# Kernel optimization log

Measured on AMD Instinct MI355X. Metric: run time of the kernel, lower is better.

Reference implementation:

```python
import jax, jax.numpy as jnp
import numpy as np

B, S, HID = 2, 2048, 2048
H, K, D = 32, 8, 64          # query heads, kv heads, head_dim
G = H // K                   # GQA group size
ROPE_MSCALE = 1.2            # constant rope_mscale applied to q and k
SM_SCALE = 1.0 / (D ** 0.5)  # flash_attn default softmax scale


def rotate_half(x):
    h = x.shape[-1] // 2
    return jnp.concatenate([-x[..., h:], x[..., :h]], axis=-1)


def setup_inputs() -> dict:
    key = jax.random.key(0)
    k1, k2, k3, k4 = jax.random.split(key, 4)
    hidden_states = jax.random.normal(k1, (B, S, HID), dtype=jnp.float32)
    # standard rotary tables: cos/sin of shape [S, D]
    inv_freq = 1.0 / (10000.0 ** (jnp.arange(0, D, 2, dtype=jnp.float32) / D))
    freqs = jnp.outer(jnp.arange(S, dtype=jnp.float32), inv_freq)  # [S, D/2]
    emb = jnp.concatenate([freqs, freqs], axis=-1)                 # [S, D]
    cos, sin = jnp.cos(emb), jnp.sin(emb)
    per_head_scale = 1.0 + 0.1 * jax.random.normal(k2, (B, H), dtype=jnp.float32)
    Wqkv = jax.random.normal(k3, ((H + 2 * K) * D, HID), dtype=jnp.float32) * (HID ** -0.5)
    Wo = jax.random.normal(k4, (HID, H * D), dtype=jnp.float32) * ((H * D) ** -0.5)
    return {"cos": cos, "sin": sin, "hidden_states": hidden_states,
            "per_head_scale": per_head_scale, "Wqkv": Wqkv, "Wo": Wo}


def reference(cos, sin, hidden_states, per_head_scale, Wqkv, Wo):
    # fused QKV projection (CastedLinear, no bias)
    qkv = jnp.einsum('bsh,oh->bso', hidden_states, Wqkv)          # [B,S,(H+2K)*D]
    qkv = qkv.reshape(B, S, H + 2 * K, D)
    q = qkv[:, :, :H]                 # [B,S,H,D]
    k = qkv[:, :, H:H + K]            # [B,S,K,D]
    v = qkv[:, :, H + K:]             # [B,S,K,D]
    # rotary embedding: cos/sin [S,D] -> broadcast over heads via [S,1,D]
    c = cos[:, None, :]
    s_ = sin[:, None, :]
    q = q * c + rotate_half(q) * s_
    k = k * c + rotate_half(k) * s_
    # rope_mscale
    q = q * ROPE_MSCALE
    k = k * ROPE_MSCALE
    # per-head scale on queries: [B,H] -> [B,1,H,1]
    q = q * per_head_scale[:, None, :, None]
    # GQA attention without materializing repeated K/V: group query heads
    qg = q.reshape(B, S, K, G, D)
    scores = jnp.einsum('bqkgd,bskd->bkgqs', qg, k) * SM_SCALE    # [B,K,G,Sq,Sk]
    causal = jnp.arange(S)[:, None] >= jnp.arange(S)[None, :]     # [Sq,Sk]
    scores = jnp.where(causal, scores, jnp.finfo(scores.dtype).min)
    probs = jax.nn.softmax(scores, axis=-1)
    out = jnp.einsum('bkgqs,bskd->bqkgd', probs, v).reshape(B, S, H * D)
    return jnp.einsum('bso,ho->bsh', out, Wo)                     # o_proj
```

## Files before the change

kernel.cpp:

```cpp
#include <hip/hip_runtime.h>
#include <stdint.h>

typedef unsigned short u16;
typedef short short8 __attribute__((ext_vector_type(8)));
typedef float f32x4 __attribute__((ext_vector_type(4)));
typedef uint32_t u32x4 __attribute__((ext_vector_type(4)));

#define S_LEN 2048
#define NQH 32
#define NKH 8
#define DHD 64
#define MNEG -1.0e30f

__device__ __forceinline__ float b2f(u16 u){
  union { uint32_t i; float f; } c; c.i = ((uint32_t)u) << 16; return c.f;
}
__device__ __forceinline__ u16 f2b(float f){
  union { float f; uint32_t i; } c; c.f = f;
  uint32_t r = c.i + 0x7fffu + ((c.i >> 16) & 1u);
  return (u16)(r >> 16);
}
__device__ __forceinline__ uint32_t cvt_pk_bf16(float lo, float hi){
  uint32_t r;
  asm("v_cvt_pk_bf16_f32 %0, %1, %2" : "=v"(r) : "v"(lo), "v"(hi));
  return r;
}
__device__ __forceinline__ void gload_lds16(const void* g, void* l){
  __builtin_amdgcn_global_load_lds((const __attribute__((address_space(1))) uint32_t*)g,
                                   (__attribute__((address_space(3))) uint32_t*)l, 16, 0, 0);
}

__global__ __launch_bounds__(256) void cvt_all(const float* __restrict__ hs,
                                               const float* __restrict__ wq,
                                               const float* __restrict__ wo,
                                               u16* __restrict__ hsB,
                                               u16* __restrict__ wqB,
                                               u16* __restrict__ woB){
  int i = blockIdx.x * 256 + threadIdx.x;
  const float* src; u16* dst; int off;
  if (i < 2097152)      { src = hs; dst = hsB; off = i; }
  else if (i < 3670016) { src = wq; dst = wqB; off = i - 2097152; }
  else                  { src = wo; dst = woB; off = i - 3670016; }
  float4 v = ((const float4*)src)[off];
  uint2 o;
  o.x = (uint32_t)f2b(v.x) | ((uint32_t)f2b(v.y) << 16);
  o.y = (uint32_t)f2b(v.z) | ((uint32_t)f2b(v.w) << 16);
  ((uint2*)dst)[off] = o;
}

template<int OUT_F32>
__global__ __launch_bounds__(256)
void gemm_bt(const u16* __restrict__ A, const u16* __restrict__ Bm,
             void* __restrict__ Cp, int N, int K)
{
  __shared__ alignas(16) u16 lA[128 * 64];
  __shared__ alignas(16) u16 lB[128 * 64];
  const int tid = threadIdx.x;
  const int w = tid >> 6, l = tid & 63;
  const int lg = l >> 4, lc = l & 15;
  const int wm = w >> 1, wn = w & 1;
  const int m0 = blockIdx.y * 128, n0 = blockIdx.x * 128;
  const int srow = l >> 3, sc = l & 7;
  const size_t ldb = (size_t)K * 2;
  f32x4 acc[4][4] = {};
  const int kiters = K >> 6;
  for (int kt = 0; kt < kiters; ++kt){
    __syncthreads();
#pragma unroll
    for (int i = 0; i < 4; ++i){
      const int row = (i * 4 + w) * 8 + srow;
      const int gc = ((sc ^ (row & 7)) << 4);
      gload_lds16((const char*)A + (size_t)(m0 + row) * ldb + (size_t)kt * 128 + gc,
                  (char*)lA + row * 128 + sc * 16);
    }
#pragma unroll
    for (int i = 0; i < 4; ++i){
      const int row = (i * 4 + w) * 8 + srow;
      const int gc = ((sc ^ (row & 7)) << 4);
      gload_lds16((const char*)Bm + (size_t)(n0 + row) * ldb + (size_t)kt * 128 + gc,
                  (char*)lB + row * 128 + sc * 16);
    }
    __syncthreads();
#pragma unroll
    for (int kk = 0; kk < 2; ++kk){
      short8 af[4], bfr[4];
#pragma unroll
      for (int mi = 0; mi < 4; ++mi){
        const int row = wm * 64 + mi * 16 + lc;
        const int cc = (kk * 4 + lg) ^ (row & 7);
        af[mi] = *(const short8*)((const char*)lA + row * 128 + cc * 16);
      }
#pragma unroll
      for (int ni = 0; ni < 4; ++ni){
        const int row = wn * 64 + ni * 16 + lc;
        const int cc = (kk * 4 + lg) ^ (row & 7);
        bfr[ni] = *(const short8*)((const char*)lB + row * 128 + cc * 16);
      }
#pragma unroll
      for (int mi = 0; mi < 4; ++mi)
#pragma unroll
        for (int ni = 0; ni < 4; ++ni)
          acc[mi][ni] = __builtin_amdgcn_mfma_f32_16x16x32_bf16(af[mi], bfr[ni], acc[mi][ni], 0, 0, 0);
    }
  }
  const int r0 = m0 + wm * 64 + lg * 4;
  const int c0 = n0 + wn * 64 + lc;
#pragma unroll
  for (int mi = 0; mi < 4; ++mi)
#pragma unroll
    for (int ni = 0; ni < 4; ++ni)
#pragma unroll
      for (int j = 0; j < 4; ++j){
        const size_t idx = (size_t)(r0 + mi * 16 + j) * (size_t)N + (size_t)(c0 + ni * 16);
        if (OUT_F32) ((float*)Cp)[idx] = acc[mi][ni][j];
        else         ((u16*)Cp)[idx]  = f2b(acc[mi][ni][j]);
      }
}

__global__ __launch_bounds__(256)
void rope_kernel(const u16* __restrict__ qkv, const float* __restrict__ cosT,
                 const float* __restrict__ sinT, const float* __restrict__ phs,
                 u16* __restrict__ Qo, u16* __restrict__ Ko)
{
  int id = blockIdx.x * 256 + threadIdx.x;
  int b = (id >= 327680) ? 1 : 0;
  int rem = id - b * 327680;
  int head = rem >> 13;
  int s = (rem >> 2) & 2047;
  int d0 = (rem & 3) << 4;
  const u16* src = qkv + (((size_t)(b * S_LEN + s) * 48 + head) << 6);
  uint4 xa = *(const uint4*)(src + d0);
  uint4 xb = *(const uint4*)(src + d0 + 8);
  int d0p = (d0 + 32) & 63;
  uint4 pa = *(const uint4*)(src + d0p);
  uint4 pb = *(const uint4*)(src + d0p + 8);
  const float* cp = cosT + s * 64 + d0;
  const float* sp = sinT + s * 64 + d0;
  const float sgn = (d0 < 32) ? -1.f : 1.f;
  const float kscale = 0.18033688011112042f;
  const float scale = (head < NQH) ? 1.2f * kscale * phs[b * NQH + head] : 1.2f;
  uint32_t xs[4] = {xa.x, xa.y, xa.z, xa.w};
  uint32_t xs2[4] = {xb.x, xb.y, xb.z, xb.w};
  uint32_t ps[4] = {pa.x, pa.y, pa.z, pa.w};
  uint32_t ps2[4] = {pb.x, pb.y, pb.z, pb.w};
  uint32_t ow[8];
#pragma unroll
  for (int k = 0; k < 4; ++k){
    float v0 = b2f((u16)(xs[k] & 0xffff)) * cp[2*k]   + sgn * b2f((u16)(ps[k] & 0xffff)) * sp[2*k];
    float v1 = b2f((u16)(xs[k] >> 16))    * cp[2*k+1] + sgn * b2f((u16)(ps[k] >> 16))    * sp[2*k+1];
    ow[k] = (uint32_t)f2b(v0 * scale) | ((uint32_t)f2b(v1 * scale) << 16);
  }
#pragma unroll
  for (int k = 0; k < 4; ++k){
    float v0 = b2f((u16)(xs2[k] & 0xffff)) * cp[8+2*k]   + sgn * b2f((u16)(ps2[k] & 0xffff)) * sp[8+2*k];
    float v1 = b2f((u16)(xs2[k] >> 16))    * cp[8+2*k+1] + sgn * b2f((u16)(ps2[k] >> 16))    * sp[8+2*k+1];
    ow[4+k] = (uint32_t)f2b(v0 * scale) | ((uint32_t)f2b(v1 * scale) << 16);
  }
  u16* dst;
  if (head < NQH) dst = Qo + (((size_t)(b * NQH + head) * S_LEN + s) << 6) + d0;
  else            dst = Ko + (((size_t)(b * NKH + head - NQH) * S_LEN + s) << 6) + d0;
  uint4 o0 = {ow[0], ow[1], ow[2], ow[3]};
  uint4 o1 = {ow[4], ow[5], ow[6], ow[7]};
  *(uint4*)dst = o0;
  *(uint4*)(dst + 8) = o1;
}

__global__ __launch_bounds__(256)
void vtrans(const u16* __restrict__ qkv, u16* __restrict__ VT)
{
  int bid = blockIdx.x;
  int st = bid & 31, kh = (bid >> 5) & 7, b = bid >> 8;
  __shared__ alignas(16) u16 t[64][72];
  int tid = threadIdx.x;
  int r = tid >> 2, c4 = tid & 3;
  const u16* src = qkv + (((size_t)(b * S_LEN + st * 64 + r) * 48 + 40 + kh) << 6) + c4 * 16;
  *(uint4*)&t[r][c4 * 16]     = *(const uint4*)src;
  *(uint4*)&t[r][c4 * 16 + 8] = *(const uint4*)(src + 8);
  __syncthreads();
  u16 o[16];
#pragma unroll
  for (int i = 0; i < 16; ++i) o[i] = t[c4 * 16 + i][r];
  u16* dst = VT + ((size_t)(b * NKH + kh) * 64 + r) * S_LEN + st * 64 + c4 * 16;
  uint4 o0 = { (uint32_t)o[0] | ((uint32_t)o[1] << 16),  (uint32_t)o[2] | ((uint32_t)o[3] << 16),
               (uint32_t)o[4] | ((uint32_t)o[5] << 16),  (uint32_t)o[6] | ((uint32_t)o[7] << 16) };
  uint4 o1 = { (uint32_t)o[8] | ((uint32_t)o[9] << 16),  (uint32_t)o[10] | ((uint32_t)o[11] << 16),
               (uint32_t)o[12] | ((uint32_t)o[13] << 16),(uint32_t)o[14] | ((uint32_t)o[15] << 16) };
  *(uint4*)dst = o0;
  *(uint4*)(dst + 8) = o1;
}

__device__ __forceinline__ void proc_chunk(f32x4 (&sv)[8], float& mrow, float& lsum,
                                           f32x4 (&o)[4], uint32_t (&pw)[4][4],
                                           const int lg, const int lc,
                                           const bool diag, const int qloc)
{
  if (diag){
#pragma unroll
    for (int nj = 0; nj < 8; ++nj)
#pragma unroll
      for (int jj = 0; jj < 4; ++jj){
        const int kloc = nj * 16 + lg * 4 + jj;
        if (kloc > qloc) sv[nj][jj] = MNEG;
      }
  }
  float mu = sv[0][0];
#pragma unroll
  for (int nj = 0; nj < 8; ++nj)
#pragma unroll
    for (int jj = 0; jj < 4; ++jj) mu = fmaxf(mu, sv[nj][jj]);
  mu = fmaxf(mu, __shfl_xor(mu, 16));
  mu = fmaxf(mu, __shfl_xor(mu, 32));
  if (!__all(mu <= mrow + 11.54f)){
    const float mnew = fmaxf(mrow, mu);
    const float sf = __builtin_amdgcn_exp2f(mrow - mnew);
    mrow = mnew;
    lsum *= sf;
#pragma unroll
    for (int dn = 0; dn < 4; ++dn)
#pragma unroll
      for (int jj = 0; jj < 4; ++jj) o[dn][jj] *= sf;
  }
  const float mcur = mrow;
  float ps = 0.f;
#pragma unroll
  for (int nj = 0; nj < 8; ++nj)
#pragma unroll
    for (int jj = 0; jj < 4; ++jj){
      const float pv = __builtin_amdgcn_exp2f(sv[nj][jj] - mcur);
      sv[nj][jj] = pv;
      ps += pv;
    }
  lsum += ps;
  uint32_t rx[8], ry[8];
#pragma unroll
  for (int nj = 0; nj < 8; ++nj){
    rx[nj] = cvt_pk_bf16(sv[nj][0], sv[nj][1]);
    ry[nj] = cvt_pk_bf16(sv[nj][2], sv[nj][3]);
  }
  const int srcA = (lg & 1) * 32 + lc;
  const bool hi = (lg & 2) != 0;
#pragma unroll
  for (int kk2 = 0; kk2 < 4; ++kk2){
    uint32_t x0 = (uint32_t)__shfl((int)rx[kk2 * 2],     srcA);
    uint32_t x1 = (uint32_t)__shfl((int)rx[kk2 * 2 + 1], srcA);
    uint32_t y0 = (uint32_t)__shfl((int)ry[kk2 * 2],     srcA);
    uint32_t y1 = (uint32_t)__shfl((int)ry[kk2 * 2 + 1], srcA);
    pw[kk2][0] = hi ? x1 : x0;
    pw[kk2][1] = hi ? y1 : y0;
    x0 = (uint32_t)__shfl((int)rx[kk2 * 2],     srcA + 16);
    x1 = (uint32_t)__shfl((int)rx[kk2 * 2 + 1], srcA + 16);
    y0 = (uint32_t)__shfl((int)ry[kk2 * 2],     srcA + 16);
    y1 = (uint32_t)__shfl((int)ry[kk2 * 2 + 1], srcA + 16);
    pw[kk2][2] = hi ? x1 : x0;
    pw[kk2][3] = hi ? y1 : y0;
  }
}

__device__ __forceinline__ short8 pw_frag(const uint32_t* pw){
  u32x4 v = { pw[0], pw[1], pw[2], pw[3] };
  return __builtin_bit_cast(short8, v);
}

__global__ __launch_bounds__(512, 2)
void attn_kernel(const u16* __restrict__ Q, const u16* __restrict__ Kr,
                 const u16* __restrict__ VT, u16* __restrict__ Ao)
{
  int bid = blockIdx.x;
  int p  = bid & 15;
  int gp = (bid >> 4) & 1;
  int kh = (bid >> 5) & 7;
  int b  = bid >> 8;
  const int qt0 = p, qt1 = 31 - p;

  __shared__ alignas(16) u16 lK[2][128 * 64];
  __shared__ alignas(16) u16 lV[2][64 * 128];

  const int tid = threadIdx.x;
  const int hh = tid >> 8;
  const int h  = kh * 4 + gp * 2 + hh;
  const int w  = (tid >> 6) & 3;
  const int l  = tid & 63;
  const int lg = l >> 4, lc = l & 15;

  short8 qf[2][2];
  {
    const u16* qbase = Q + ((size_t)(b * NQH + h) * S_LEN) * 64;
#pragma unroll
    for (int kk = 0; kk < 2; ++kk){
      qf[0][kk] = *(const short8*)(qbase + (size_t)(qt0 * 64 + w * 16 + lc) * 64 + kk * 32 + lg * 8);
      qf[1][kk] = *(const short8*)(qbase + (size_t)(qt1 * 64 + w * 16 + lc) * 64 + kk * 32 + lg * 8);
    }
  }

  const u16* Kb = Kr + (size_t)(b * NKH + kh) * S_LEN * 64;
  const u16* Vb = VT + (size_t)(b * NKH + kh) * 64 * S_LEN;

  f32x4 o[2][4] = {};
  float mrow[2] = {MNEG, MNEG};
  float lsum[2] = {0.f, 0.f};

  const int nt = (qt1 >> 1) + 1;
  const int nt0 = qt0 >> 1;

#define STAGE(T, BSEL) do { \
    _Pragma("unroll") \
    for (int i_ = 0; i_ < 2; ++i_){ \
      const int row_ = i_ * 64 + (tid >> 3); \
      const int ch_  = tid & 7; \
      const int gc_  = ((ch_ ^ (row_ & 7)) << 4); \
      gload_lds16((const char*)(Kb + (size_t)((T) * 128 + row_) * 64) + gc_, \
                  (char*)lK[BSEL] + row_ * 128 + ch_ * 16); \
    } \
    _Pragma("unroll") \
    for (int i_ = 0; i_ < 2; ++i_){ \
      const int row_ = i_ * 32 + (tid >> 4); \
      const int ch_  = tid & 15; \
      const int gc_  = ((ch_ ^ (row_ & 15)) << 4); \
      gload_lds16((const char*)(Vb + (size_t)row_ * S_LEN + (T) * 128) + gc_, \
                  (char*)lV[BSEL] + row_ * 256 + ch_ * 16); \
    } \
  } while (0)

  STAGE(0, 0);

  for (int t = 0; t < nt; ++t){
    const int cur = t & 1;
    const bool act0 = (t <= nt0);
    if (t + 1 < nt){
      STAGE(t + 1, cur ^ 1);
      asm volatile("s_waitcnt vmcnt(4)" ::: "memory");
    } else {
      asm volatile("s_waitcnt vmcnt(0)" ::: "memory");
    }
    __builtin_amdgcn_s_barrier();

    f32x4 sv[2][8] = {};
    __builtin_amdgcn_s_setprio(1);
#pragma unroll
    for (int kk = 0; kk < 2; ++kk){
      short8 kf[8];
#pragma unroll
      for (int nj = 0; nj < 8; ++nj){
        const int row = nj * 16 + lc;
        const int cc = (kk * 4 + lg) ^ (row & 7);
        kf[nj] = *(const short8*)((const char*)lK[cur] + row * 128 + cc * 16);
      }
      if (act0)
#pragma unroll
        for (int nj = 0; nj < 8; ++nj)
          sv[0][nj] = __builtin_amdgcn_mfma_f32_16x16x32_bf16(kf[nj], qf[0][kk], sv[0][nj], 0, 0, 0);
#pragma unroll
      for (int nj = 0; nj < 8; ++nj)
        sv[1][nj] = __builtin_amdgcn_mfma_f32_16x16x32_bf16(kf[nj], qf[1][kk], sv[1][nj], 0, 0, 0);
    }
    __builtin_amdgcn_s_setprio(0);

    uint32_t pw[2][4][4];
    if (act0)
      proc_chunk(sv[0], mrow[0], lsum[0], o[0], pw[0], lg, lc,
                 t == (qt0 >> 1), (qt0 & 1) * 64 + w * 16 + lc);
    proc_chunk(sv[1], mrow[1], lsum[1], o[1], pw[1], lg, lc,
               t == (qt1 >> 1), (qt1 & 1) * 64 + w * 16 + lc);

    __builtin_amdgcn_s_setprio(1);
#pragma unroll
    for (int kk2 = 0; kk2 < 4; ++kk2){
      short8 vf[4];
#pragma unroll
      for (int dn = 0; dn < 4; ++dn){
        const int row = dn * 16 + lc;
        const int cc = (kk2 * 4 + lg) ^ (row & 15);
        vf[dn] = *(const short8*)((const char*)lV[cur] + row * 256 + cc * 16);
      }
      if (act0){
        const short8 pb0 = pw_frag(pw[0][kk2]);
#pragma unroll
        for (int dn = 0; dn < 4; ++dn)
          o[0][dn] = __builtin_amdgcn_mfma_f32_16x16x32_bf16(vf[dn], pb0, o[0][dn], 0, 0, 0);
      }
      const short8 pb1 = pw_frag(pw[1][kk2]);
#pragma unroll
      for (int dn = 0; dn < 4; ++dn)
        o[1][dn] = __builtin_amdgcn_mfma_f32_16x16x32_bf16(vf[dn], pb1, o[1][dn], 0, 0, 0);
    }
    __builtin_amdgcn_s_setprio(0);
    __builtin_amdgcn_s_barrier();
  }
#undef STAGE

#pragma unroll
  for (int c = 0; c < 2; ++c){
    const int qt = c ? qt1 : qt0;
    float ls = lsum[c];
    ls += __shfl_xor(ls, 16);
    ls += __shfl_xor(ls, 32);
    const float inv = 1.f / ls;
    const int sq = qt * 64 + w * 16 + lc;
#pragma unroll
    for (int dn = 0; dn < 4; ++dn){
      uint2 pk;
      pk.x = cvt_pk_bf16(o[c][dn][0] * inv, o[c][dn][1] * inv);
      pk.y = cvt_pk_bf16(o[c][dn][2] * inv, o[c][dn][3] * inv);
      const int col = h * 64 + dn * 16 + lg * 4;
      *(uint2*)&Ao[(size_t)(b * S_LEN + sq) * 2048 + col] = pk;
    }
  }
}

extern "C" void kernel_launch(void* const* d_in, const int* in_sizes, int n_in,
                              void* d_out, int out_size, void* d_ws, size_t ws_size,
                              hipStream_t stream)
{
  const float* cosT = (const float*)d_in[0];
  const float* sinT = (const float*)d_in[1];
  const float* hs   = (const float*)d_in[2];
  const float* phs  = (const float*)d_in[3];
  const float* Wqkv = (const float*)d_in[4];
  const float* Wo   = (const float*)d_in[5];
  float* out = (float*)d_out;
  char* ws = (char*)d_ws;

  u16* hsB   = (u16*)(ws);
  u16* WqkvB = (u16*)(ws + 16777216);
  u16* WoB   = (u16*)(ws + 29360128);
  u16* qkvB  = (u16*)(ws + 37748736);
  u16* Qb    = (u16*)(ws + 62914560);
  u16* Kb    = (u16*)(ws + 79691776);
  u16* VTb   = (u16*)(ws + 83886080);
  u16* Ao    = hsB;

  cvt_all<<<18432, 256, 0, stream>>>(hs, Wqkv, Wo, hsB, WqkvB, WoB);
  gemm_bt<0><<<dim3(24, 32), 256, 0, stream>>>(hsB, WqkvB, (void*)qkvB, 3072, 2048);
  rope_kernel<<<2560, 256, 0, stream>>>(qkvB, cosT, sinT, phs, Qb, Kb);
  vtrans<<<512, 256, 0, stream>>>(qkvB, VTb);
  attn_kernel<<<512, 512, 0, stream>>>(Qb, Kb, VTb, Ao);
  gemm_bt<1><<<dim3(16, 32), 256, 0, stream>>>(Ao, WoB, (void*)out, 2048, 2048);
}
```

Baseline: 237.6 us.

## Permute V^T key order to match P register layout, drop shuffles

The V transpose kernel now handles 128-key tiles and writes keys in a permuted order that matches the lane layout the softmax probabilities already have in registers. The attention inner loop then packs P to bf16 directly instead of doing 16 cross-lane shuffles per chunk. This removes shuffle and select work from the hot attention loop. The cost is a more complex, coordinated layout in the transpose kernel, and correctness depends on the permutation matching the MFMA fragment mapping exactly.

```diff
diff --git a/kernel.cpp b/kernel.cpp
--- a/kernel.cpp
+++ b/kernel.cpp
@@ -169,24 +169,36 @@
 void vtrans(const u16* __restrict__ qkv, u16* __restrict__ VT)
 {
   int bid = blockIdx.x;
-  int st = bid & 31, kh = (bid >> 5) & 7, b = bid >> 8;
-  __shared__ alignas(16) u16 t[64][72];
+  int t = bid & 15, kh = (bid >> 4) & 7, b = bid >> 7;
+  __shared__ u16 vlds[128][72];
   int tid = threadIdx.x;
-  int r = tid >> 2, c4 = tid & 3;
-  const u16* src = qkv + (((size_t)(b * S_LEN + st * 64 + r) * 48 + 40 + kh) << 6) + c4 * 16;
-  *(uint4*)&t[r][c4 * 16]     = *(const uint4*)src;
-  *(uint4*)&t[r][c4 * 16 + 8] = *(const uint4*)(src + 8);
+  {
+    int r = tid >> 1, half = tid & 1;
+    const u16* src = qkv + (((size_t)(b * S_LEN + t * 128 + r) * 48 + 40 + kh) << 6) + half * 32;
+    uint4 a0 = *(const uint4*)(src);
+    uint4 a1 = *(const uint4*)(src + 8);
+    uint4 a2 = *(const uint4*)(src + 16);
+    uint4 a3 = *(const uint4*)(src + 24);
+    *(uint4*)&vlds[r][half * 32]      = a0;
+    *(uint4*)&vlds[r][half * 32 + 8]  = a1;
+    *(uint4*)&vlds[r][half * 32 + 16] = a2;
+    *(uint4*)&vlds[r][half * 32 + 24] = a3;
+  }
   __syncthreads();
-  u16 o[16];
-#pragma unroll
-  for (int i = 0; i < 16; ++i) o[i] = t[c4 * 16 + i][r];
-  u16* dst = VT + ((size_t)(b * NKH + kh) * 64 + r) * S_LEN + st * 64 + c4 * 16;
-  uint4 o0 = { (uint32_t)o[0] | ((uint32_t)o[1] << 16),  (uint32_t)o[2] | ((uint32_t)o[3] << 16),
-               (uint32_t)o[4] | ((uint32_t)o[5] << 16),  (uint32_t)o[6] | ((uint32_t)o[7] << 16) };
-  uint4 o1 = { (uint32_t)o[8] | ((uint32_t)o[9] << 16),  (uint32_t)o[10] | ((uint32_t)o[11] << 16),
-               (uint32_t)o[12] | ((uint32_t)o[13] << 16),(uint32_t)o[14] | ((uint32_t)o[15] << 16) };
-  *(uint4*)dst = o0;
-  *(uint4*)(dst + 8) = o1;
+  const int d = tid >> 2, kk2 = tid & 3;
+  u16* dst = VT + ((size_t)(b * NKH + kh) * 64 + d) * S_LEN + t * 128 + kk2 * 32;
+#pragma unroll
+  for (int j = 0; j < 4; ++j){
+    u16 o[8];
+#pragma unroll
+    for (int e = 0; e < 8; ++e){
+      const int hk = kk2 * 32 + ((e >> 2) << 4) + j * 4 + (e & 3);
+      o[e] = vlds[hk][d];
+    }
+    uint4 ov = { (uint32_t)o[0] | ((uint32_t)o[1] << 16), (uint32_t)o[2] | ((uint32_t)o[3] << 16),
+                 (uint32_t)o[4] | ((uint32_t)o[5] << 16), (uint32_t)o[6] | ((uint32_t)o[7] << 16) };
+    *(uint4*)(dst + j * 8) = ov;
+  }
 }
 
 __device__ __forceinline__ void proc_chunk(f32x4 (&sv)[8], float& mrow, float& lsum,
@@ -231,28 +243,12 @@
       ps += pv;
     }
   lsum += ps;
-  uint32_t rx[8], ry[8];
-#pragma unroll
-  for (int nj = 0; nj < 8; ++nj){
-    rx[nj] = cvt_pk_bf16(sv[nj][0], sv[nj][1]);
-    ry[nj] = cvt_pk_bf16(sv[nj][2], sv[nj][3]);
-  }
-  const int srcA = (lg & 1) * 32 + lc;
-  const bool hi = (lg & 2) != 0;
 #pragma unroll
   for (int kk2 = 0; kk2 < 4; ++kk2){
-    uint32_t x0 = (uint32_t)__shfl((int)rx[kk2 * 2],     srcA);
-    uint32_t x1 = (uint32_t)__shfl((int)rx[kk2 * 2 + 1], srcA);
-    uint32_t y0 = (uint32_t)__shfl((int)ry[kk2 * 2],     srcA);
-    uint32_t y1 = (uint32_t)__shfl((int)ry[kk2 * 2 + 1], srcA);
-    pw[kk2][0] = hi ? x1 : x0;
-    pw[kk2][1] = hi ? y1 : y0;
-    x0 = (uint32_t)__shfl((int)rx[kk2 * 2],     srcA + 16);
-    x1 = (uint32_t)__shfl((int)rx[kk2 * 2 + 1], srcA + 16);
-    y0 = (uint32_t)__shfl((int)ry[kk2 * 2],     srcA + 16);
-    y1 = (uint32_t)__shfl((int)ry[kk2 * 2 + 1], srcA + 16);
-    pw[kk2][2] = hi ? x1 : x0;
-    pw[kk2][3] = hi ? y1 : y0;
+    pw[kk2][0] = cvt_pk_bf16(sv[kk2 * 2][0],     sv[kk2 * 2][1]);
+    pw[kk2][1] = cvt_pk_bf16(sv[kk2 * 2][2],     sv[kk2 * 2][3]);
+    pw[kk2][2] = cvt_pk_bf16(sv[kk2 * 2 + 1][0], sv[kk2 * 2 + 1][1]);
+    pw[kk2][3] = cvt_pk_bf16(sv[kk2 * 2 + 1][2], sv[kk2 * 2 + 1][3]);
   }
 }
 
@@ -432,7 +428,7 @@
   cvt_all<<<18432, 256, 0, stream>>>(hs, Wqkv, Wo, hsB, WqkvB, WoB);
   gemm_bt<0><<<dim3(24, 32), 256, 0, stream>>>(hsB, WqkvB, (void*)qkvB, 3072, 2048);
   rope_kernel<<<2560, 256, 0, stream>>>(qkvB, cosT, sinT, phs, Qb, Kb);
-  vtrans<<<512, 256, 0, stream>>>(qkvB, VTb);
+  vtrans<<<256, 256, 0, stream>>>(qkvB, VTb);
   attn_kernel<<<512, 512, 0, stream>>>(Qb, Kb, VTb, Ao);
   gemm_bt<1><<<dim3(16, 32), 256, 0, stream>>>(Ao, WoB, (void*)out, 2048, 2048);
 }
```

Result: faster. 223.7 us (-5.8%).
